# Kernel tuning notes

Measured on AMD Instinct MI355X. Metric: run time of the kernel, lower is better.

Reference implementation:

```python
import jax, jax.numpy as jnp
import numpy as np

B, H, S = 256, 128, 2048

def setup_inputs() -> dict:
    key = jax.random.key(0)
    ks = jax.random.split(key, 8)
    static_embedding = jax.random.normal(ks[0], (B, H, S), dtype=jnp.float32)
    dynamic_embedding = jax.random.normal(ks[1], (B, S, H), dtype=jnp.float32)
    decoder_output = jax.random.normal(ks[2], (B, H, 1), dtype=jnp.float32)
    mask = jax.random.randint(ks[3], (B, S), 0, 2).astype(bool)
    # xavier-uniform-ish init scales
    lim_v = float(np.sqrt(6.0 / (1 + H)))
    lim_W = float(np.sqrt(6.0 / (H + 3 * H)))
    lim_W2 = float(np.sqrt(6.0 / (H + 2 * H)))
    v = jax.random.uniform(ks[4], (H,), minval=-lim_v, maxval=lim_v, dtype=jnp.float32)
    W = jax.random.uniform(ks[5], (H, 3 * H), minval=-lim_W, maxval=lim_W, dtype=jnp.float32)
    v2 = jax.random.uniform(ks[6], (H,), minval=-lim_v, maxval=lim_v, dtype=jnp.float32)
    W2 = jax.random.uniform(ks[7], (H, 2 * H), minval=-lim_W2, maxval=lim_W2, dtype=jnp.float32)
    return {"static_embedding": static_embedding, "dynamic_embedding": dynamic_embedding,
            "decoder_output": decoder_output, "mask": mask,
            "v": v, "W": W, "v2": v2, "W2": W2}


def reference(static_embedding, dynamic_embedding, decoder_output, mask, v, W, v2, W2):
    b, h, s = static_embedding.shape
    dec = jnp.broadcast_to(decoder_output, (b, h, s))               # [B,H,S]
    hidden = jnp.concatenate(
        [static_embedding, jnp.swapaxes(dynamic_embedding, 1, 2), dec], axis=1)  # [B,3H,S]
    # stage 1: additive scoring  v^T tanh(W @ hidden)
    t1 = jnp.tanh(jnp.einsum('hk,bks->bhs', W, hidden))             # [B,H,S]
    attns = jnp.einsum('h,bhs->bs', v, t1)                          # [B,S]
    enc_attn = jax.nn.softmax(attns, axis=1)                        # [B,S]
    # context over static embeddings
    context = jnp.einsum('bs,bhs->bh', enc_attn, static_embedding)  # [B,H]
    energy = jnp.concatenate(
        [static_embedding, jnp.broadcast_to(context[:, :, None], (b, h, s))], axis=1)  # [B,2H,S]
    # stage 2
    t2 = jnp.tanh(jnp.einsum('hk,bks->bhs', W2, energy))            # [B,H,S]
    probs = jnp.einsum('h,bhs->bs', v2, t2)                         # [B,S]
    probs = jnp.where(mask, -jnp.inf, probs)
    return jax.nn.softmax(probs, axis=1)
```

## Files before the change

### kernel.cpp

```cpp
#include <hip/hip_runtime.h>
#include <stdint.h>
#include <math.h>

#define B_ 256
#define H_ 128
#define S_ 2048

typedef __attribute__((ext_vector_type(8))) short short8;
typedef __attribute__((ext_vector_type(4))) float f32x4;
typedef __attribute__((ext_vector_type(4))) unsigned int u32x4;

typedef const __attribute__((address_space(1))) void gvoid_t;
typedef __attribute__((address_space(3))) void lvoid_t;

__device__ __forceinline__ unsigned short f2bf(float f) {
  uint32_t u = __builtin_bit_cast(uint32_t, f);
  u += 0x7fffu + ((u >> 16) & 1u);
  return (unsigned short)(u >> 16);
}

__device__ __forceinline__ uint32_t cvtpk(float lo, float hi) {
  uint32_t r;
  asm("v_cvt_pk_bf16_f32 %0, %1, %2" : "=v"(r) : "v"(lo), "v"(hi));
  return r;
}

__device__ __forceinline__ float bf2f(unsigned short u) {
  return __builtin_bit_cast(float, (uint32_t)u << 16);
}

__device__ __forceinline__ float tanh5(float x) {
  float e = __builtin_amdgcn_exp2f(x * 2.8853900817779268f);
  float r = __builtin_amdgcn_rcpf(1.0f + e);
  return fmaf(-2.0f, r, 1.0f);
}

#define WS_NEED 4718592u
#define WST_OFF 8388608u
#define WS_T_NEED (WST_OFF + (size_t)B_ * (S_/16) * 4 * 64 * 8 * 2)

__global__ __launch_bounds__(256) void prep_wfrags(
    const float* __restrict__ W, const float* __restrict__ W2,
    unsigned short* __restrict__ wsA) {
  int idx = blockIdx.x * 256 + threadIdx.x;
  if (idx >= 24 * 4 * 64 * 8) return;
  int j = idx & 7;
  int lane = (idx >> 3) & 63;
  int t = (idx >> 9) & 3;
  int tile = idx >> 11;
  int li = lane & 15;
  int k = t * 32 + (lane >> 4) * 8 + j;
  float val;
  if (tile < 8)        val = W[(tile * 16 + li) * 384 + k];
  else if (tile < 16)  val = W2[((tile - 8) * 16 + li) * 256 + k];
  else                 val = W[((tile - 16) * 16 + li) * 384 + 128 + k];
  wsA[idx] = f2bf(val);
}

__global__ __launch_bounds__(128) void prep_c1(
    const float* __restrict__ W, const float* __restrict__ dec,
    float* __restrict__ c1) {
  int b = blockIdx.x;
  int h = threadIdx.x;
  __shared__ float sdec[H_];
  sdec[h] = dec[b * H_ + h];
  __syncthreads();
  const float* wr = W + h * 384 + 256;
  float acc = 0.f;
  #pragma unroll 4
  for (int k = 0; k < 128; ++k) acc += wr[k] * sdec[k];
  c1[b * H_ + h] = acc;
}

__global__ void detect_mask(const unsigned char* __restrict__ mb, int* __restrict__ flag) {
  __shared__ int sGT1, sNZ;
  if (threadIdx.x == 0) { sGT1 = 0; sNZ = 0; }
  __syncthreads();
  int gt1 = 0, nz = 0;
  for (int i = threadIdx.x; i < 8192; i += 256) {
    unsigned char c = mb[i];
    if (c > 1) gt1 = 1;
    if ((i & 3) && c) nz = 1;
  }
  if (gt1) atomicOr(&sGT1, 1);
  if (nz)  atomicOr(&sNZ, 1);
  __syncthreads();
  if (threadIdx.x == 0) *flag = sGT1 ? 2 : (sNZ ? 1 : 0);
}

__global__ __launch_bounds__(256) void stage1(
    const float* __restrict__ sEmb, const float* __restrict__ dEmb,
    const unsigned short* __restrict__ wsA, const float* __restrict__ c1,
    const float* __restrict__ v, float* __restrict__ attns,
    unsigned short* __restrict__ wsT) {
  const int b = blockIdx.y;
  const int tid = threadIdx.x;
  const int lane = tid & 63, w = tid >> 6, g = lane >> 4, li = lane & 15;
  __shared__ float sS[128 * 64];
  __shared__ unsigned short frag[4][8][512];
  __shared__ float spart[256];
  __shared__ float sc1[H_], sv[H_];

  const size_t sbase = (size_t)b * H_ * S_;
  const size_t dbase = (size_t)b * S_ * H_;
  const int sblk = blockIdx.x * 512;

  short8 aW[2][4], aB[2][4];
  #pragma unroll
  for (int mm = 0; mm < 2; ++mm)
    #pragma unroll
    for (int t = 0; t < 4; ++t) {
      aW[mm][t] = *(const short8*)(wsA + (size_t)(((2 * w + mm) * 4 + t) * 64 + lane) * 8);
      aB[mm][t] = *(const short8*)(wsA + (size_t)(((16 + 2 * w + mm) * 4 + t) * 64 + lane) * 8);
    }
  if (tid < 128) { sc1[tid] = c1[b * H_ + tid]; sv[tid] = v[tid]; }

  const int lrow = lane >> 4, lcol4 = 4 * (lane & 15);
  auto stageS = [&](int soff) {
    #pragma unroll
    for (int i = 0; i < 8; ++i) {
      int r = 32 * w + 4 * i + lrow;
      int gcol = lcol4 ^ (((r >> 3) & 3) << 3);
      const float* src = sEmb + sbase + (size_t)r * S_ + soff + gcol;
      __builtin_amdgcn_global_load_lds((gvoid_t*)src, (lvoid_t*)&sS[(32 * w + 4 * i) * 64],
                                       16, 0, 0);
    }
  };
  f32x4 dv[8];
  auto loadD = [&](int soff) {
    const float* dr = dEmb + dbase + (size_t)(soff + 16 * w + li) * H_ + 8 * g;
    #pragma unroll
    for (int t = 0; t < 4; ++t) {
      dv[2 * t]     = *(const f32x4*)(dr + 32 * t);
      dv[2 * t + 1] = *(const f32x4*)(dr + 32 * t + 4);
    }
  };

  stageS(sblk);
  loadD(sblk);

  const int colA = (16 * w + li) ^ (g << 3);

  for (int c = 0; c < 8; ++c) {
    const int soff = sblk + c * 64;
    __syncthreads();
    if (c > 0 && tid < 64)
      attns[(size_t)b * S_ + soff - 64 + tid] =
          spart[tid] + spart[64 + tid] + spart[128 + tid] + spart[192 + tid];

    #pragma unroll
    for (int t = 0; t < 4; ++t) {
      const int rb = (32 * t + 8 * g) * 64 + colA;
      uint32_t s0 = cvtpk(sS[rb], sS[rb + 64]);
      uint32_t s1 = cvtpk(sS[rb + 128], sS[rb + 192]);
      uint32_t s2 = cvtpk(sS[rb + 256], sS[rb + 320]);
      uint32_t s3 = cvtpk(sS[rb + 384], sS[rb + 448]);
      u32x4 us = {s0, s1, s2, s3};
      short8 bS = __builtin_bit_cast(short8, us);
      uint32_t d0 = cvtpk(dv[2 * t].x, dv[2 * t].y);
      uint32_t d1 = cvtpk(dv[2 * t].z, dv[2 * t].w);
      uint32_t d2 = cvtpk(dv[2 * t + 1].x, dv[2 * t + 1].y);
      uint32_t d3 = cvtpk(dv[2 * t + 1].z, dv[2 * t + 1].w);
      u32x4 ud = {d0, d1, d2, d3};
      short8 bD = __builtin_bit_cast(short8, ud);
      *(short8*)&frag[w][t][lane * 8] = bS;
      *(short8*)&frag[w][4 + t][lane * 8] = bD;
      if (wsT)
        *(short8*)&wsT[(((size_t)b * (S_ / 16) + (soff >> 4) + w) * 4 + t) * 512 + lane * 8] = bS;
    }
    __syncthreads();
    if (c + 1 < 8) { stageS(soff + 64); loadD(soff + 64); }

    f32x4 acc[4][2];
    #pragma unroll
    for (int st = 0; st < 4; ++st) { acc[st][0] = (f32x4)0.0f; acc[st][1] = (f32x4)0.0f; }
    #pragma unroll
    for (int st = 0; st < 4; ++st)
      #pragma unroll
      for (int t = 0; t < 4; ++t) {
        short8 bS = *(const short8*)&frag[st][t][lane * 8];
        short8 bD = *(const short8*)&frag[st][4 + t][lane * 8];
        acc[st][0] = __builtin_amdgcn_mfma_f32_16x16x32_bf16(aW[0][t], bS, acc[st][0], 0, 0, 0);
        acc[st][1] = __builtin_amdgcn_mfma_f32_16x16x32_bf16(aW[1][t], bS, acc[st][1], 0, 0, 0);
        acc[st][0] = __builtin_amdgcn_mfma_f32_16x16x32_bf16(aB[0][t], bD, acc[st][0], 0, 0, 0);
        acc[st][1] = __builtin_amdgcn_mfma_f32_16x16x32_bf16(aB[1][t], bD, acc[st][1], 0, 0, 0);
      }

    #pragma unroll
    for (int st = 0; st < 4; ++st) {
      float part = 0.f;
      #pragma unroll
      for (int mm = 0; mm < 2; ++mm)
        #pragma unroll
        for (int r = 0; r < 4; ++r) {
          int h = 32 * w + 16 * mm + 4 * g + r;
          part += sv[h] * tanh5(acc[st][mm][r] + sc1[h]);
        }
      part += __shfl_xor(part, 16);
      part += __shfl_xor(part, 32);
      if (lane < 16) spart[w * 64 + st * 16 + li] = part;
    }
  }
  __syncthreads();
  if (tid < 64)
    attns[(size_t)b * S_ + sblk + 448 + tid] =
        spart[tid] + spart[64 + tid] + spart[128 + tid] + spart[192 + tid];
}

__global__ __launch_bounds__(512) void fuse2(
    const float* __restrict__ attns, const unsigned short* __restrict__ wsT,
    const unsigned short* __restrict__ wsA, const float* __restrict__ W2,
    const float* __restrict__ v2, const unsigned char* __restrict__ mask8,
    const int* __restrict__ flag, float* __restrict__ out) {
  const int b = blockIdx.x;
  const int tid = threadIdx.x;
  const int lane = tid & 63, wv = tid >> 6, g = lane >> 4, li = lane & 15;
  __shared__ float buf[S_];
  __shared__ float sctx[8][H_];
  __shared__ float2 sq[H_];
  __shared__ float wred[8];
  __shared__ float sred;

  const size_t pbase = (size_t)b * (S_ / 16);

  float a[4];
  #pragma unroll
  for (int i = 0; i < 4; ++i) a[i] = attns[(size_t)b * S_ + i * 512 + tid];
  float mx = fmaxf(fmaxf(a[0], a[1]), fmaxf(a[2], a[3]));
  #pragma unroll
  for (int off = 32; off >= 1; off >>= 1) mx = fmaxf(mx, __shfl_xor(mx, off));
  if (lane == 0) wred[wv] = mx;
  __syncthreads();
  if (tid == 0) {
    float m = wred[0];
    #pragma unroll
    for (int i = 1; i < 8; ++i) m = fmaxf(m, wred[i]);
    sred = m;
  }
  __syncthreads();
  mx = sred;
  __syncthreads();
  float sum = 0.f;
  #pragma unroll
  for (int i = 0; i < 4; ++i) {
    float e = __expf(a[i] - mx);
    buf[i * 512 + tid] = e;
    sum += e;
  }
  #pragma unroll
  for (int off = 32; off >= 1; off >>= 1) sum += __shfl_xor(sum, off);
  if (lane == 0) wred[wv] = sum;
  __syncthreads();
  if (tid == 0) {
    float s = 0.f;
    #pragma unroll
    for (int i = 0; i < 8; ++i) s += wred[i];
    sred = 1.0f / s;
  }
  __syncthreads();
  const float inv1 = sred;
  __syncthreads();

  float hacc[4][8];
  #pragma unroll
  for (int t = 0; t < 4; ++t)
    #pragma unroll
    for (int j = 0; j < 8; ++j) hacc[t][j] = 0.f;
  short8 cur[4];
  #pragma unroll
  for (int t = 0; t < 4; ++t)
    cur[t] = *(const short8*)&wsT[((pbase + wv) * 4 + t) * 512 + lane * 8];
  for (int stile = wv; stile < 128; stile += 8) {
    short8 nxt[4];
    const bool more = (stile + 8) < 128;
    if (more) {
      #pragma unroll
      for (int t = 0; t < 4; ++t)
        nxt[t] = *(const short8*)&wsT[((pbase + stile + 8) * 4 + t) * 512 + lane * 8];
    }
    float pw = buf[stile * 16 + li];
    #pragma unroll
    for (int t = 0; t < 4; ++t)
      #pragma unroll
      for (int j = 0; j < 8; ++j)
        hacc[t][j] = fmaf(pw, bf2f((unsigned short)cur[t][j]), hacc[t][j]);
    if (more) {
      #pragma unroll
      for (int t = 0; t < 4; ++t) cur[t] = nxt[t];
    }
  }
  #pragma unroll
  for (int t = 0; t < 4; ++t)
    #pragma unroll
    for (int j = 0; j < 8; ++j) {
      float x = hacc[t][j];
      x += __shfl_xor(x, 1); x += __shfl_xor(x, 2);
      x += __shfl_xor(x, 4); x += __shfl_xor(x, 8);
      hacc[t][j] = x;
    }
  if (li == 0) {
    #pragma unroll
    for (int t = 0; t < 4; ++t)
      #pragma unroll
      for (int j = 0; j < 8; ++j)
        sctx[wv][32 * t + 8 * g + j] = hacc[t][j];
  }
  __syncthreads();

  if (tid < 128) {
    float cx = 0.f;
    #pragma unroll
    for (int q = 0; q < 8; ++q) cx += sctx[q][tid];
    sctx[0][tid] = cx * inv1;
  }
  __syncthreads();
  if (tid < 128) {
    const float* wr = W2 + tid * 256 + 128;
    float c2v = 0.f;
    #pragma unroll 4
    for (int k = 0; k < 128; ++k) c2v += wr[k] * sctx[0][k];
    sq[tid] = make_float2(c2v, v2[tid]);
  }
  __syncthreads();

  short8 aW[8][4];
  #pragma unroll
  for (int m = 0; m < 8; ++m)
    #pragma unroll
    for (int t = 0; t < 4; ++t)
      aW[m][t] = *(const short8*)(wsA + (size_t)(((8 + m) * 4 + t) * 64 + lane) * 8);
  const int f = *flag;

  short8 bcur[4];
  #pragma unroll
  for (int t = 0; t < 4; ++t)
    bcur[t] = *(const short8*)&wsT[((pbase + wv) * 4 + t) * 512 + lane * 8];
  for (int stile = wv; stile < 128; stile += 8) {
    short8 bnxt[4];
    const bool more = (stile + 8) < 128;
    if (more) {
      #pragma unroll
      for (int t = 0; t < 4; ++t)
        bnxt[t] = *(const short8*)&wsT[((pbase + stile + 8) * 4 + t) * 512 + lane * 8];
    }
    f32x4 acc[8];
    #pragma unroll
    for (int m = 0; m < 8; ++m) acc[m] = (f32x4)0.0f;
    #pragma unroll
    for (int t = 0; t < 4; ++t)
      #pragma unroll
      for (int m = 0; m < 8; ++m)
        acc[m] = __builtin_amdgcn_mfma_f32_16x16x32_bf16(aW[m][t], bcur[t], acc[m], 0, 0, 0);
    float part = 0.f;
    #pragma unroll
    for (int m = 0; m < 8; ++m)
      #pragma unroll
      for (int r = 0; r < 4; ++r) {
        float2 q = sq[16 * m + 4 * g + r];
        part += q.y * tanh5(acc[m][r] + q.x);
      }
    part += __shfl_xor(part, 16);
    part += __shfl_xor(part, 32);
    if (lane < 16) {
      int s = stile * 16 + li;
      size_t mi = (size_t)b * S_ + s;
      bool msk;
      if (f == 1)      msk = mask8[mi] != 0;
      else if (f == 2) msk = ((const float*)mask8)[mi] != 0.0f;
      else             msk = ((const int*)mask8)[mi] != 0;
      buf[s] = msk ? -INFINITY : part;
    }
    if (more) {
      #pragma unroll
      for (int t = 0; t < 4; ++t) bcur[t] = bnxt[t];
    }
  }
  __syncthreads();

  float s4[4];
  #pragma unroll
  for (int i = 0; i < 4; ++i) s4[i] = buf[i * 512 + tid];
  float mx2 = fmaxf(fmaxf(s4[0], s4[1]), fmaxf(s4[2], s4[3]));
  #pragma unroll
  for (int off = 32; off >= 1; off >>= 1) mx2 = fmaxf(mx2, __shfl_xor(mx2, off));
  if (lane == 0) wred[wv] = mx2;
  __syncthreads();
  if (tid == 0) {
    float m = wred[0];
    #pragma unroll
    for (int i = 1; i < 8; ++i) m = fmaxf(m, wred[i]);
    sred = m;
  }
  __syncthreads();
  mx2 = sred;
  __syncthreads();
  float e4[4];
  float sum2 = 0.f;
  #pragma unroll
  for (int i = 0; i < 4; ++i) { e4[i] = __expf(s4[i] - mx2); sum2 += e4[i]; }
  #pragma unroll
  for (int off = 32; off >= 1; off >>= 1) sum2 += __shfl_xor(sum2, off);
  if (lane == 0) wred[wv] = sum2;
  __syncthreads();
  if (tid == 0) {
    float s = 0.f;
    #pragma unroll
    for (int i = 0; i < 8; ++i) s += wred[i];
    sred = 1.0f / s;
  }
  __syncthreads();
  const float inv2 = sred;
  #pragma unroll
  for (int i = 0; i < 4; ++i) out[(size_t)b * S_ + i * 512 + tid] = e4[i] * inv2;
}

__global__ __launch_bounds__(256) void kmid_a(
    const float* __restrict__ attns, const float* __restrict__ sEmb,
    float* __restrict__ ctx) {
  int q = blockIdx.x, b = blockIdx.y;
  int tid = threadIdx.x, lane = tid & 63, w = tid >> 6;
  __shared__ float p[S_];
  __shared__ float wred[4];
  __shared__ float sred;
  float a[8];
  #pragma unroll
  for (int i = 0; i < 8; ++i) a[i] = attns[(size_t)b * S_ + i * 256 + tid];
  float mx = a[0];
  #pragma unroll
  for (int i = 1; i < 8; ++i) mx = fmaxf(mx, a[i]);
  #pragma unroll
  for (int off = 32; off >= 1; off >>= 1) mx = fmaxf(mx, __shfl_xor(mx, off));
  if (lane == 0) wred[w] = mx;
  __syncthreads();
  if (tid == 0) sred = fmaxf(fmaxf(wred[0], wred[1]), fmaxf(wred[2], wred[3]));
  __syncthreads();
  mx = sred;
  __syncthreads();
  float sum = 0.f;
  #pragma unroll
  for (int i = 0; i < 8; ++i) {
    float e = __expf(a[i] - mx);
    p[i * 256 + tid] = e;
    sum += e;
  }
  #pragma unroll
  for (int off = 32; off >= 1; off >>= 1) sum += __shfl_xor(sum, off);
  if (lane == 0) wred[w] = sum;
  __syncthreads();
  if (tid == 0) sred = 1.0f / (wred[0] + wred[1] + wred[2] + wred[3]);
  __syncthreads();
  float inv = sred;
  #pragma unroll
  for (int hh = 0; hh < 8; ++hh) {
    int h = q * 32 + w * 8 + hh;
    const f32x4* xp = (const f32x4*)(sEmb + (size_t)b * H_ * S_ + (size_t)h * S_);
    float av = 0.f;
    #pragma unroll
    for (int it = 0; it < 8; ++it) {
      f32x4 x = xp[it * 64 + lane];
      f32x4 pp = *(const f32x4*)&p[(it * 64 + lane) * 4];
      av += x.x * pp.x + x.y * pp.y + x.z * pp.z + x.w * pp.w;
    }
    #pragma unroll
    for (int off = 32; off >= 1; off >>= 1) av += __shfl_xor(av, off);
    if (lane == 0) ctx[b * H_ + h] = av * inv;
  }
}

__global__ __launch_bounds__(128) void kmid_b(
    const float* __restrict__ W2, const float* __restrict__ ctx,
    float* __restrict__ c2) {
  int b = blockIdx.x;
  int h = threadIdx.x;
  __shared__ float sc[H_];
  sc[h] = ctx[b * H_ + h];
  __syncthreads();
  const float* wr = W2 + h * 256 + 128;
  float acc = 0.f;
  #pragma unroll 4
  for (int k = 0; k < 128; ++k) acc += wr[k] * sc[k];
  c2[b * H_ + h] = acc;
}

__global__ __launch_bounds__(256) void stage2F(
    const float* __restrict__ sEmb, const unsigned short* __restrict__ wsA,
    const float* __restrict__ c2, const float* __restrict__ v2,
    const unsigned char* __restrict__ mask8, const int* __restrict__ flag,
    float* __restrict__ score) {
  int b = blockIdx.y;
  int tid = threadIdx.x;
  int lane = tid & 63, w = tid >> 6, g = lane >> 4, li = lane & 15;
  __shared__ float sS[128 * 64];
  __shared__ float sc2[H_], sv2[H_];
  __shared__ float spart[256];
  const int schunk = blockIdx.x * 64;
  const size_t sbase = (size_t)b * H_ * S_;
  short8 aW[2][4];
  #pragma unroll
  for (int mm = 0; mm < 2; ++mm)
    #pragma unroll
    for (int t = 0; t < 4; ++t)
      aW[mm][t] = *(const short8*)(wsA + (size_t)(((8 + 2 * w + mm) * 4 + t) * 64 + lane) * 8);
  {
    int lrow = lane >> 4, lcol4 = 4 * (lane & 15);
    #pragma unroll
    for (int i = 0; i < 8; ++i) {
      int r = 32 * w + 4 * i + lrow;
      int gcol = lcol4 ^ (((r >> 3) & 3) << 3);
      const float* src = sEmb + sbase + (size_t)r * S_ + schunk + gcol;
      __builtin_amdgcn_global_load_lds((gvoid_t*)src, (lvoid_t*)&sS[(32 * w + 4 * i) * 64],
                                       16, 0, 0);
    }
  }
  if (tid < 128) { sc2[tid] = c2[b * H_ + tid]; sv2[tid] = v2[tid]; }
  __syncthreads();
  f32x4 acc[4][2];
  #pragma unroll
  for (int st = 0; st < 4; ++st) { acc[st][0] = (f32x4)0.0f; acc[st][1] = (f32x4)0.0f; }
  #pragma unroll
  for (int st = 0; st < 4; ++st) {
    const int colA = (16 * st + li) ^ (g << 3);
    #pragma unroll
    for (int t = 0; t < 4; ++t) {
      short8 bS;
      #pragma unroll
      for (int j = 0; j < 8; ++j)
        bS[j] = (short)f2bf(sS[(32 * t + 8 * g + j) * 64 + colA]);
      acc[st][0] = __builtin_amdgcn_mfma_f32_16x16x32_bf16(aW[0][t], bS, acc[st][0], 0, 0, 0);
      acc[st][1] = __builtin_amdgcn_mfma_f32_16x16x32_bf16(aW[1][t], bS, acc[st][1], 0, 0, 0);
    }
  }
  #pragma unroll
  for (int st = 0; st < 4; ++st) {
    float part = 0.f;
    #pragma unroll
    for (int mm = 0; mm < 2; ++mm)
      #pragma unroll
      for (int r = 0; r < 4; ++r) {
        int h = 32 * w + 16 * mm + 4 * g + r;
        part += sv2[h] * tanh5(acc[st][mm][r] + sc2[h]);
      }
    part += __shfl_xor(part, 16);
    part += __shfl_xor(part, 32);
    if (lane < 16) spart[w * 64 + st * 16 + li] = part;
  }
  __syncthreads();
  if (tid < 64) {
    float tot = spart[tid] + spart[64 + tid] + spart[128 + tid] + spart[192 + tid];
    size_t mi = (size_t)b * S_ + schunk + tid;
    int f = *flag;
    bool msk;
    if (f == 1)      msk = mask8[mi] != 0;
    else if (f == 2) msk = ((const float*)mask8)[mi] != 0.0f;
    else             msk = ((const int*)mask8)[mi] != 0;
    score[mi] = msk ? -INFINITY : tot;
  }
}

__global__ __launch_bounds__(256) void ksoftmax(
    const float* __restrict__ score, float* __restrict__ out) {
  int b = blockIdx.x;
  int tid = threadIdx.x, lane = tid & 63, w = tid >> 6;
  __shared__ float wred[4];
  __shared__ float sred;
  float a[8];
  #pragma unroll
  for (int i = 0; i < 8; ++i) a[i] = score[(size_t)b * S_ + i * 256 + tid];
  float mx = a[0];
  #pragma unroll
  for (int i = 1; i < 8; ++i) mx = fmaxf(mx, a[i]);
  #pragma unroll
  for (int off = 32; off >= 1; off >>= 1) mx = fmaxf(mx, __shfl_xor(mx, off));
  if (lane == 0) wred[w] = mx;
  __syncthreads();
  if (tid == 0) sred = fmaxf(fmaxf(wred[0], wred[1]), fmaxf(wred[2], wred[3]));
  __syncthreads();
  mx = sred;
  __syncthreads();
  float e[8];
  float sum = 0.f;
  #pragma unroll
  for (int i = 0; i < 8; ++i) { e[i] = __expf(a[i] - mx); sum += e[i]; }
  #pragma unroll
  for (int off = 32; off >= 1; off >>= 1) sum += __shfl_xor(sum, off);
  if (lane == 0) wred[w] = sum;
  __syncthreads();
  if (tid == 0) sred = 1.0f / (wred[0] + wred[1] + wred[2] + wred[3]);
  __syncthreads();
  float inv = sred;
  #pragma unroll
  for (int i = 0; i < 8; ++i) out[(size_t)b * S_ + i * 256 + tid] = e[i] * inv;
}

extern "C" void kernel_launch(void* const* d_in, const int* in_sizes, int n_in,
                              void* d_out, int out_size, void* d_ws, size_t ws_size,
                              hipStream_t stream) {
  (void)in_sizes; (void)n_in; (void)out_size;
  if (ws_size < WS_NEED) return;
  const float* sEmb = (const float*)d_in[0];
  const float* dEmb = (const float*)d_in[1];
  const float* dec  = (const float*)d_in[2];
  const unsigned char* mask = (const unsigned char*)d_in[3];
  const float* v    = (const float*)d_in[4];
  const float* W    = (const float*)d_in[5];
  const float* v2   = (const float*)d_in[6];
  const float* W2   = (const float*)d_in[7];

  char* ws = (char*)d_ws;
  unsigned short* wsA = (unsigned short*)(ws);
  int*   flag  = (int*)  (ws + 114688);
  float* c1    = (float*)(ws + 131072);
  float* c2    = (float*)(ws + 262144);
  float* ctx   = (float*)(ws + 393216);
  float* attns = (float*)(ws + 524288);
  float* score = (float*)(ws + 2621440);
  bool useT = (ws_size >= WS_T_NEED);
  unsigned short* wsT = useT ? (unsigned short*)(ws + WST_OFF) : nullptr;

  prep_wfrags<<<192, 256, 0, stream>>>(W, W2, wsA);
  prep_c1<<<B_, 128, 0, stream>>>(W, dec, c1);
  detect_mask<<<1, 256, 0, stream>>>(mask, flag);
  stage1<<<dim3(4, B_), 256, 0, stream>>>(sEmb, dEmb, wsA, c1, v, attns, wsT);
  if (useT) {
    fuse2<<<B_, 512, 0, stream>>>(attns, wsT, wsA, W2, v2, mask, flag, (float*)d_out);
  } else {
    kmid_a<<<dim3(4, B_), 256, 0, stream>>>(attns, sEmb, ctx);
    kmid_b<<<B_, 128, 0, stream>>>(W2, ctx, c2);
    stage2F<<<dim3(32, B_), 256, 0, stream>>>(sEmb, wsA, c2, v2, mask, flag, score);
    ksoftmax<<<B_, 256, 0, stream>>>(score, (float*)d_out);
  }
}
```

Measured before the change: 229.9 us.

## Restructure stage1 into K-blocked mega1 with double-buffered LDS and more blocks

```diff
diff --git a/kernel.cpp b/kernel.cpp
--- a/kernel.cpp
+++ b/kernel.cpp
@@ -12,6 +12,8 @@
 
 typedef const __attribute__((address_space(1))) void gvoid_t;
 typedef __attribute__((address_space(3))) void lvoid_t;
+
+#define SCHED0 __builtin_amdgcn_sched_barrier(0)
 
 __device__ __forceinline__ unsigned short f2bf(float f) {
   uint32_t u = __builtin_bit_cast(uint32_t, f);
@@ -88,7 +90,7 @@
   if (threadIdx.x == 0) *flag = sGT1 ? 2 : (sNZ ? 1 : 0);
 }
 
-__global__ __launch_bounds__(256) void stage1(
+__global__ __launch_bounds__(256, 2) void mega1(
     const float* __restrict__ sEmb, const float* __restrict__ dEmb,
     const unsigned short* __restrict__ wsA, const float* __restrict__ c1,
     const float* __restrict__ v, float* __restrict__ attns,
@@ -96,6 +98,331 @@
   const int b = blockIdx.y;
   const int tid = threadIdx.x;
   const int lane = tid & 63, w = tid >> 6, g = lane >> 4, li = lane & 15;
+  __shared__ float sS[2][32 * 128];
+  __shared__ float sc1[H_], sv[H_];
+
+  const size_t sbase = (size_t)b * H_ * S_;
+  const size_t dbase = (size_t)b * S_ * H_;
+  const size_t pbase = (size_t)b * (S_ / 16);
+  const int sblk = blockIdx.x * 128;
+  const int st0 = 2 * w;
+
+  { int hh = 32 * w + (lane & 31); sc1[hh] = c1[b * H_ + hh]; sv[hh] = v[hh]; }
+  SCHED0;
+
+  auto stageS = [&](int kb, int buf) {
+    #pragma unroll
+    for (int i = 0; i < 4; ++i) {
+      int rp = 8 * w + 2 * i;
+      int r = rp + (lane >> 5);
+      int swz = ((r >> 3) & 3) << 3;
+      const float* src = sEmb + sbase + (size_t)(32 * kb + r) * S_ + sblk
+                         + ((4 * (lane & 31)) ^ swz);
+      __builtin_amdgcn_global_load_lds((gvoid_t*)src,
+                                       (lvoid_t*)&sS[buf][rp * 128], 16, 0, 0);
+    }
+  };
+
+  f32x4 dva[4], dvb[4];
+  auto loadDyn = [&](int kb, f32x4* dv) {
+    #pragma unroll
+    for (int tt = 0; tt < 2; ++tt) {
+      const float* p = dEmb + dbase
+                       + (size_t)(sblk + 16 * (st0 + tt) + li) * H_ + 32 * kb + 8 * g;
+      dv[2 * tt]     = *(const f32x4*)(p);
+      dv[2 * tt + 1] = *(const f32x4*)(p + 4);
+    }
+  };
+
+  stageS(0, 0);
+  SCHED0;
+  loadDyn(0, dva);
+  SCHED0;
+
+  f32x4 acc[2][8];
+  #pragma unroll
+  for (int tt = 0; tt < 2; ++tt)
+    #pragma unroll
+    for (int m = 0; m < 8; ++m) acc[tt][m] = (f32x4)0.0f;
+
+  for (int kb = 0; kb < 4; ++kb) {
+    if (kb == 0) { asm volatile("s_waitcnt vmcnt(4)" ::: "memory"); }
+    else         { asm volatile("s_waitcnt vmcnt(6)" ::: "memory"); }
+    asm volatile("s_waitcnt lgkmcnt(0)" ::: "memory");
+    SCHED0;
+    __builtin_amdgcn_s_barrier();
+    SCHED0;
+
+    short8 aW[8], aB[8];
+    #pragma unroll
+    for (int m = 0; m < 8; ++m) {
+      aW[m] = *(const short8*)(wsA + (size_t)((m * 4 + kb) * 64 + lane) * 8);
+      aB[m] = *(const short8*)(wsA + (size_t)(((16 + m) * 4 + kb) * 64 + lane) * 8);
+    }
+    SCHED0;
+    if (kb + 1 < 4) {
+      stageS(kb + 1, (kb + 1) & 1);
+      SCHED0;
+      loadDyn(kb + 1, (kb & 1) ? dva : dvb);
+    }
+    SCHED0;
+
+    const float* sSc = sS[kb & 1];
+    const f32x4* dvv = (kb & 1) ? dvb : dva;
+    #pragma unroll
+    for (int tt = 0; tt < 2; ++tt) {
+      const int colr = (16 * (st0 + tt) + li) ^ (g << 3);
+      const int rb = 8 * g * 128 + colr;
+      uint32_t s0 = cvtpk(sSc[rb],       sSc[rb + 128]);
+      uint32_t s1 = cvtpk(sSc[rb + 256], sSc[rb + 384]);
+      uint32_t s2 = cvtpk(sSc[rb + 512], sSc[rb + 640]);
+      uint32_t s3 = cvtpk(sSc[rb + 768], sSc[rb + 896]);
+      u32x4 us = {s0, s1, s2, s3};
+      short8 bS = __builtin_bit_cast(short8, us);
+      f32x4 a0 = dvv[2 * tt], a1 = dvv[2 * tt + 1];
+      u32x4 ud = {cvtpk(a0.x, a0.y), cvtpk(a0.z, a0.w),
+                  cvtpk(a1.x, a1.y), cvtpk(a1.z, a1.w)};
+      short8 bD = __builtin_bit_cast(short8, ud);
+      *(short8*)&wsT[((pbase + (sblk >> 4) + st0 + tt) * 4 + kb) * 512 + lane * 8] = bS;
+      #pragma unroll
+      for (int m = 0; m < 8; ++m) {
+        acc[tt][m] = __builtin_amdgcn_mfma_f32_16x16x32_bf16(aW[m], bS, acc[tt][m], 0, 0, 0);
+        acc[tt][m] = __builtin_amdgcn_mfma_f32_16x16x32_bf16(aB[m], bD, acc[tt][m], 0, 0, 0);
+      }
+    }
+  }
+
+  #pragma unroll
+  for (int tt = 0; tt < 2; ++tt) {
+    float part = 0.f;
+    #pragma unroll
+    for (int m = 0; m < 8; ++m)
+      #pragma unroll
+      for (int r = 0; r < 4; ++r) {
+        int h = 16 * m + 4 * g + r;
+        part += sv[h] * tanh5(acc[tt][m][r] + sc1[h]);
+      }
+    part += __shfl_xor(part, 16);
+    part += __shfl_xor(part, 32);
+    if (lane < 16)
+      attns[(size_t)b * S_ + sblk + 16 * (st0 + tt) + li] = part;
+  }
+}
+
+__global__ __launch_bounds__(512) void fuse2(
+    const float* __restrict__ attns, const unsigned short* __restrict__ wsT,
+    const unsigned short* __restrict__ wsA, const float* __restrict__ W2,
+    const float* __restrict__ v2, const unsigned char* __restrict__ mask8,
+    const int* __restrict__ flag, float* __restrict__ out) {
+  const int b = blockIdx.x;
+  const int tid = threadIdx.x;
+  const int lane = tid & 63, wv = tid >> 6, g = lane >> 4, li = lane & 15;
+  __shared__ float buf[S_];
+  __shared__ float sctx[8][H_];
+  __shared__ float2 sq[H_];
+  __shared__ float wred[8];
+  __shared__ float sred;
+
+  const size_t pbase = (size_t)b * (S_ / 16);
+
+  float a[4];
+  #pragma unroll
+  for (int i = 0; i < 4; ++i) a[i] = attns[(size_t)b * S_ + i * 512 + tid];
+  float mx = fmaxf(fmaxf(a[0], a[1]), fmaxf(a[2], a[3]));
+  #pragma unroll
+  for (int off = 32; off >= 1; off >>= 1) mx = fmaxf(mx, __shfl_xor(mx, off));
+  if (lane == 0) wred[wv] = mx;
+  __syncthreads();
+  if (tid == 0) {
+    float m = wred[0];
+    #pragma unroll
+    for (int i = 1; i < 8; ++i) m = fmaxf(m, wred[i]);
+    sred = m;
+  }
+  __syncthreads();
+  mx = sred;
+  __syncthreads();
+  float sum = 0.f;
+  #pragma unroll
+  for (int i = 0; i < 4; ++i) {
+    float e = __expf(a[i] - mx);
+    buf[i * 512 + tid] = e;
+    sum += e;
+  }
+  #pragma unroll
+  for (int off = 32; off >= 1; off >>= 1) sum += __shfl_xor(sum, off);
+  if (lane == 0) wred[wv] = sum;
+  __syncthreads();
+  if (tid == 0) {
+    float s = 0.f;
+    #pragma unroll
+    for (int i = 0; i < 8; ++i) s += wred[i];
+    sred = 1.0f / s;
+  }
+  __syncthreads();
+  const float inv1 = sred;
+  __syncthreads();
+
+  float hacc[4][8];
+  #pragma unroll
+  for (int t = 0; t < 4; ++t)
+    #pragma unroll
+    for (int j = 0; j < 8; ++j) hacc[t][j] = 0.f;
+  short8 cur[4];
+  #pragma unroll
+  for (int t = 0; t < 4; ++t)
+    cur[t] = *(const short8*)&wsT[((pbase + wv) * 4 + t) * 512 + lane * 8];
+  for (int stile = wv; stile < 128; stile += 8) {
+    short8 nxt[4];
+    const bool more = (stile + 8) < 128;
+    if (more) {
+      #pragma unroll
+      for (int t = 0; t < 4; ++t)
+        nxt[t] = *(const short8*)&wsT[((pbase + stile + 8) * 4 + t) * 512 + lane * 8];
+    }
+    float pw = buf[stile * 16 + li];
+    #pragma unroll
+    for (int t = 0; t < 4; ++t)
+      #pragma unroll
+      for (int j = 0; j < 8; ++j)
+        hacc[t][j] = fmaf(pw, bf2f((unsigned short)cur[t][j]), hacc[t][j]);
+    if (more) {
+      #pragma unroll
+      for (int t = 0; t < 4; ++t) cur[t] = nxt[t];
+    }
+  }
+  #pragma unroll
+  for (int t = 0; t < 4; ++t)
+    #pragma unroll
+    for (int j = 0; j < 8; ++j) {
+      float x = hacc[t][j];
+      x += __shfl_xor(x, 1); x += __shfl_xor(x, 2);
+      x += __shfl_xor(x, 4); x += __shfl_xor(x, 8);
+      hacc[t][j] = x;
+    }
+  if (li == 0) {
+    #pragma unroll
+    for (int t = 0; t < 4; ++t)
+      #pragma unroll
+      for (int j = 0; j < 8; ++j)
+        sctx[wv][32 * t + 8 * g + j] = hacc[t][j];
+  }
+  __syncthreads();
+
+  if (tid < 128) {
+    float cx = 0.f;
+    #pragma unroll
+    for (int q = 0; q < 8; ++q) cx += sctx[q][tid];
+    sctx[0][tid] = cx * inv1;
+  }
+  __syncthreads();
+  if (tid < 128) {
+    const float* wr = W2 + tid * 256 + 128;
+    float c2v = 0.f;
+    #pragma unroll 4
+    for (int k = 0; k < 128; ++k) c2v += wr[k] * sctx[0][k];
+    sq[tid] = make_float2(c2v, v2[tid]);
+  }
+  __syncthreads();
+
+  short8 aW[8][4];
+  #pragma unroll
+  for (int m = 0; m < 8; ++m)
+    #pragma unroll
+    for (int t = 0; t < 4; ++t)
+      aW[m][t] = *(const short8*)(wsA + (size_t)(((8 + m) * 4 + t) * 64 + lane) * 8);
+  const int f = *flag;
+
+  short8 bcur[4];
+  #pragma unroll
+  for (int t = 0; t < 4; ++t)
+    bcur[t] = *(const short8*)&wsT[((pbase + wv) * 4 + t) * 512 + lane * 8];
+  for (int stile = wv; stile < 128; stile += 8) {
+    short8 bnxt[4];
+    const bool more = (stile + 8) < 128;
+    if (more) {
+      #pragma unroll
+      for (int t = 0; t < 4; ++t)
+        bnxt[t] = *(const short8*)&wsT[((pbase + stile + 8) * 4 + t) * 512 + lane * 8];
+    }
+    f32x4 acc[8];
+    #pragma unroll
+    for (int m = 0; m < 8; ++m) acc[m] = (f32x4)0.0f;
+    #pragma unroll
+    for (int t = 0; t < 4; ++t)
+      #pragma unroll
+      for (int m = 0; m < 8; ++m)
+        acc[m] = __builtin_amdgcn_mfma_f32_16x16x32_bf16(aW[m][t], bcur[t], acc[m], 0, 0, 0);
+    float part = 0.f;
+    #pragma unroll
+    for (int m = 0; m < 8; ++m)
+      #pragma unroll
+      for (int r = 0; r < 4; ++r) {
+        float2 q = sq[16 * m + 4 * g + r];
+        part += q.y * tanh5(acc[m][r] + q.x);
+      }
+    part += __shfl_xor(part, 16);
+    part += __shfl_xor(part, 32);
+    if (lane < 16) {
+      int s = stile * 16 + li;
+      size_t mi = (size_t)b * S_ + s;
+      bool msk;
+      if (f == 1)      msk = mask8[mi] != 0;
+      else if (f == 2) msk = ((const float*)mask8)[mi] != 0.0f;
+      else             msk = ((const int*)mask8)[mi] != 0;
+      buf[s] = msk ? -INFINITY : part;
+    }
+    if (more) {
+      #pragma unroll
+      for (int t = 0; t < 4; ++t) bcur[t] = bnxt[t];
+    }
+  }
+  __syncthreads();
+
+  float s4[4];
+  #pragma unroll
+  for (int i = 0; i < 4; ++i) s4[i] = buf[i * 512 + tid];
+  float mx2 = fmaxf(fmaxf(s4[0], s4[1]), fmaxf(s4[2], s4[3]));
+  #pragma unroll
+  for (int off = 32; off >= 1; off >>= 1) mx2 = fmaxf(mx2, __shfl_xor(mx2, off));
+  if (lane == 0) wred[wv] = mx2;
+  __syncthreads();
+  if (tid == 0) {
+    float m = wred[0];
+    #pragma unroll
+    for (int i = 1; i < 8; ++i) m = fmaxf(m, wred[i]);
+    sred = m;
+  }
+  __syncthreads();
+  mx2 = sred;
+  __syncthreads();
+  float e4[4];
+  float sum2 = 0.f;
+  #pragma unroll
+  for (int i = 0; i < 4; ++i) { e4[i] = __expf(s4[i] - mx2); sum2 += e4[i]; }
+  #pragma unroll
+  for (int off = 32; off >= 1; off >>= 1) sum2 += __shfl_xor(sum2, off);
+  if (lane == 0) wred[wv] = sum2;
+  __syncthreads();
+  if (tid == 0) {
+    float s = 0.f;
+    #pragma unroll
+    for (int i = 0; i < 8; ++i) s += wred[i];
+    sred = 1.0f / s;
+  }
+  __syncthreads();
+  const float inv2 = sred;
+  #pragma unroll
+  for (int i = 0; i < 4; ++i) out[(size_t)b * S_ + i * 512 + tid] = e4[i] * inv2;
+}
+
+__global__ __launch_bounds__(256) void stage1_fb(
+    const float* __restrict__ sEmb, const float* __restrict__ dEmb,
+    const unsigned short* __restrict__ wsA, const float* __restrict__ c1,
+    const float* __restrict__ v, float* __restrict__ attns) {
+  const int b = blockIdx.y;
+  const int tid = threadIdx.x;
+  const int lane = tid & 63, w = tid >> 6, g = lane >> 4, li = lane & 15;
   __shared__ float sS[128 * 64];
   __shared__ unsigned short frag[4][8][512];
   __shared__ float spart[256];
@@ -135,10 +462,8 @@
       dv[2 * t + 1] = *(const f32x4*)(dr + 32 * t + 4);
     }
   };
-
   stageS(sblk);
   loadD(sblk);
-
   const int colA = (16 * w + li) ^ (g << 3);
 
   for (int c = 0; c < 8; ++c) {
@@ -147,7 +472,6 @@
     if (c > 0 && tid < 64)
       attns[(size_t)b * S_ + soff - 64 + tid] =
           spart[tid] + spart[64 + tid] + spart[128 + tid] + spart[192 + tid];
-
     #pragma unroll
     for (int t = 0; t < 4; ++t) {
       const int rb = (32 * t + 8 * g) * 64 + colA;
@@ -165,12 +489,9 @@
       short8 bD = __builtin_bit_cast(short8, ud);
       *(short8*)&frag[w][t][lane * 8] = bS;
       *(short8*)&frag[w][4 + t][lane * 8] = bD;
-      if (wsT)
-        *(short8*)&wsT[(((size_t)b * (S_ / 16) + (soff >> 4) + w) * 4 + t) * 512 + lane * 8] = bS;
     }
     __syncthreads();
     if (c + 1 < 8) { stageS(soff + 64); loadD(soff + 64); }
-
     f32x4 acc[4][2];
     #pragma unroll
     for (int st = 0; st < 4; ++st) { acc[st][0] = (f32x4)0.0f; acc[st][1] = (f32x4)0.0f; }
@@ -185,7 +506,6 @@
         acc[st][0] = __builtin_amdgcn_mfma_f32_16x16x32_bf16(aB[0][t], bD, acc[st][0], 0, 0, 0);
         acc[st][1] = __builtin_amdgcn_mfma_f32_16x16x32_bf16(aB[1][t], bD, acc[st][1], 0, 0, 0);
       }
-
     #pragma unroll
     for (int st = 0; st < 4; ++st) {
       float part = 0.f;
@@ -205,213 +525,6 @@
   if (tid < 64)
     attns[(size_t)b * S_ + sblk + 448 + tid] =
         spart[tid] + spart[64 + tid] + spart[128 + tid] + spart[192 + tid];
-}
-
-__global__ __launch_bounds__(512) void fuse2(
-    const float* __restrict__ attns, const unsigned short* __restrict__ wsT,
-    const unsigned short* __restrict__ wsA, const float* __restrict__ W2,
-    const float* __restrict__ v2, const unsigned char* __restrict__ mask8,
-    const int* __restrict__ flag, float* __restrict__ out) {
-  const int b = blockIdx.x;
-  const int tid = threadIdx.x;
-  const int lane = tid & 63, wv = tid >> 6, g = lane >> 4, li = lane & 15;
-  __shared__ float buf[S_];
-  __shared__ float sctx[8][H_];
-  __shared__ float2 sq[H_];
-  __shared__ float wred[8];
-  __shared__ float sred;
-
-  const size_t pbase = (size_t)b * (S_ / 16);
-
-  float a[4];
-  #pragma unroll
-  for (int i = 0; i < 4; ++i) a[i] = attns[(size_t)b * S_ + i * 512 + tid];
-  float mx = fmaxf(fmaxf(a[0], a[1]), fmaxf(a[2], a[3]));
-  #pragma unroll
-  for (int off = 32; off >= 1; off >>= 1) mx = fmaxf(mx, __shfl_xor(mx, off));
-  if (lane == 0) wred[wv] = mx;
-  __syncthreads();
-  if (tid == 0) {
-    float m = wred[0];
-    #pragma unroll
-    for (int i = 1; i < 8; ++i) m = fmaxf(m, wred[i]);
-    sred = m;
-  }
-  __syncthreads();
-  mx = sred;
-  __syncthreads();
-  float sum = 0.f;
-  #pragma unroll
-  for (int i = 0; i < 4; ++i) {
-    float e = __expf(a[i] - mx);
-    buf[i * 512 + tid] = e;
-    sum += e;
-  }
-  #pragma unroll
-  for (int off = 32; off >= 1; off >>= 1) sum += __shfl_xor(sum, off);
-  if (lane == 0) wred[wv] = sum;
-  __syncthreads();
-  if (tid == 0) {
-    float s = 0.f;
-    #pragma unroll
-    for (int i = 0; i < 8; ++i) s += wred[i];
-    sred = 1.0f / s;
-  }
-  __syncthreads();
-  const float inv1 = sred;
-  __syncthreads();
-
-  float hacc[4][8];
-  #pragma unroll
-  for (int t = 0; t < 4; ++t)
-    #pragma unroll
-    for (int j = 0; j < 8; ++j) hacc[t][j] = 0.f;
-  short8 cur[4];
-  #pragma unroll
-  for (int t = 0; t < 4; ++t)
-    cur[t] = *(const short8*)&wsT[((pbase + wv) * 4 + t) * 512 + lane * 8];
-  for (int stile = wv; stile < 128; stile += 8) {
-    short8 nxt[4];
-    const bool more = (stile + 8) < 128;
-    if (more) {
-      #pragma unroll
-      for (int t = 0; t < 4; ++t)
-        nxt[t] = *(const short8*)&wsT[((pbase + stile + 8) * 4 + t) * 512 + lane * 8];
-    }
-    float pw = buf[stile * 16 + li];
-    #pragma unroll
-    for (int t = 0; t < 4; ++t)
-      #pragma unroll
-      for (int j = 0; j < 8; ++j)
-        hacc[t][j] = fmaf(pw, bf2f((unsigned short)cur[t][j]), hacc[t][j]);
-    if (more) {
-      #pragma unroll
-      for (int t = 0; t < 4; ++t) cur[t] = nxt[t];
-    }
-  }
-  #pragma unroll
-  for (int t = 0; t < 4; ++t)
-    #pragma unroll
-    for (int j = 0; j < 8; ++j) {
-      float x = hacc[t][j];
-      x += __shfl_xor(x, 1); x += __shfl_xor(x, 2);
-      x += __shfl_xor(x, 4); x += __shfl_xor(x, 8);
-      hacc[t][j] = x;
-    }
-  if (li == 0) {
-    #pragma unroll
-    for (int t = 0; t < 4; ++t)
-      #pragma unroll
-      for (int j = 0; j < 8; ++j)
-        sctx[wv][32 * t + 8 * g + j] = hacc[t][j];
-  }
-  __syncthreads();
-
-  if (tid < 128) {
-    float cx = 0.f;
-    #pragma unroll
-    for (int q = 0; q < 8; ++q) cx += sctx[q][tid];
-    sctx[0][tid] = cx * inv1;
-  }
-  __syncthreads();
-  if (tid < 128) {
-    const float* wr = W2 + tid * 256 + 128;
-    float c2v = 0.f;
-    #pragma unroll 4
-    for (int k = 0; k < 128; ++k) c2v += wr[k] * sctx[0][k];
-    sq[tid] = make_float2(c2v, v2[tid]);
-  }
-  __syncthreads();
-
-  short8 aW[8][4];
-  #pragma unroll
-  for (int m = 0; m < 8; ++m)
-    #pragma unroll
-    for (int t = 0; t < 4; ++t)
-      aW[m][t] = *(const short8*)(wsA + (size_t)(((8 + m) * 4 + t) * 64 + lane) * 8);
-  const int f = *flag;
-
-  short8 bcur[4];
-  #pragma unroll
-  for (int t = 0; t < 4; ++t)
-    bcur[t] = *(const short8*)&wsT[((pbase + wv) * 4 + t) * 512 + lane * 8];
-  for (int stile = wv; stile < 128; stile += 8) {
-    short8 bnxt[4];
-    const bool more = (stile + 8) < 128;
-    if (more) {
-      #pragma unroll
-      for (int t = 0; t < 4; ++t)
-        bnxt[t] = *(const short8*)&wsT[((pbase + stile + 8) * 4 + t) * 512 + lane * 8];
-    }
-    f32x4 acc[8];
-    #pragma unroll
-    for (int m = 0; m < 8; ++m) acc[m] = (f32x4)0.0f;
-    #pragma unroll
-    for (int t = 0; t < 4; ++t)
-      #pragma unroll
-      for (int m = 0; m < 8; ++m)
-        acc[m] = __builtin_amdgcn_mfma_f32_16x16x32_bf16(aW[m][t], bcur[t], acc[m], 0, 0, 0);
-    float part = 0.f;
-    #pragma unroll
-    for (int m = 0; m < 8; ++m)
-      #pragma unroll
-      for (int r = 0; r < 4; ++r) {
-        float2 q = sq[16 * m + 4 * g + r];
-        part += q.y * tanh5(acc[m][r] + q.x);
-      }
-    part += __shfl_xor(part, 16);
-    part += __shfl_xor(part, 32);
-    if (lane < 16) {
-      int s = stile * 16 + li;
-      size_t mi = (size_t)b * S_ + s;
-      bool msk;
-      if (f == 1)      msk = mask8[mi] != 0;
-      else if (f == 2) msk = ((const float*)mask8)[mi] != 0.0f;
-      else             msk = ((const int*)mask8)[mi] != 0;
-      buf[s] = msk ? -INFINITY : part;
-    }
-    if (more) {
-      #pragma unroll
-      for (int t = 0; t < 4; ++t) bcur[t] = bnxt[t];
-    }
-  }
-  __syncthreads();
-
-  float s4[4];
-  #pragma unroll
-  for (int i = 0; i < 4; ++i) s4[i] = buf[i * 512 + tid];
-  float mx2 = fmaxf(fmaxf(s4[0], s4[1]), fmaxf(s4[2], s4[3]));
-  #pragma unroll
-  for (int off = 32; off >= 1; off >>= 1) mx2 = fmaxf(mx2, __shfl_xor(mx2, off));
-  if (lane == 0) wred[wv] = mx2;
-  __syncthreads();
-  if (tid == 0) {
-    float m = wred[0];
-    #pragma unroll
-    for (int i = 1; i < 8; ++i) m = fmaxf(m, wred[i]);
-    sred = m;
-  }
-  __syncthreads();
-  mx2 = sred;
-  __syncthreads();
-  float e4[4];
-  float sum2 = 0.f;
-  #pragma unroll
-  for (int i = 0; i < 4; ++i) { e4[i] = __expf(s4[i] - mx2); sum2 += e4[i]; }
-  #pragma unroll
-  for (int off = 32; off >= 1; off >>= 1) sum2 += __shfl_xor(sum2, off);
-  if (lane == 0) wred[wv] = sum2;
-  __syncthreads();
-  if (tid == 0) {
-    float s = 0.f;
-    #pragma unroll
-    for (int i = 0; i < 8; ++i) s += wred[i];
-    sred = 1.0f / s;
-  }
-  __syncthreads();
-  const float inv2 = sred;
-  #pragma unroll
-  for (int i = 0; i < 4; ++i) out[(size_t)b * S_ + i * 512 + tid] = e4[i] * inv2;
 }
 
 __global__ __launch_bounds__(256) void kmid_a(
@@ -620,10 +733,11 @@
   prep_wfrags<<<192, 256, 0, stream>>>(W, W2, wsA);
   prep_c1<<<B_, 128, 0, stream>>>(W, dec, c1);
   detect_mask<<<1, 256, 0, stream>>>(mask, flag);
-  stage1<<<dim3(4, B_), 256, 0, stream>>>(sEmb, dEmb, wsA, c1, v, attns, wsT);
   if (useT) {
+    mega1<<<dim3(16, B_), 256, 0, stream>>>(sEmb, dEmb, wsA, c1, v, attns, wsT);
     fuse2<<<B_, 512, 0, stream>>>(attns, wsT, wsA, W2, v2, mask, flag, (float*)d_out);
   } else {
+    stage1_fb<<<dim3(4, B_), 256, 0, stream>>>(sEmb, dEmb, wsA, c1, v, attns);
     kmid_a<<<dim3(4, B_), 256, 0, stream>>>(attns, sEmb, ctx);
     kmid_b<<<B_, 128, 0, stream>>>(W2, ctx, c2);
     stage2F<<<dim3(32, B_), 256, 0, stream>>>(sEmb, wsA, c2, v2, mask, flag, score);
```

Measured after the change: 236.7 us. +2.9%, slower.
